# Kernel tuning notes

Hardware: AMD Instinct MI355X
Metric: run time of the kernel (lower is better)

Reference implementation:

```python
import jax, jax.numpy as jnp
import numpy as np

B, N, D = 8, 1024, 512
H, DH = 8, 64          # num_heads, dim_head_output
MLP = 2048
PRUNE_NUM = 64         # remove_num > 0 -> prune branch of determine_fuse
KEEP_NUM = 3
NEG = -1e10


def setup_inputs() -> dict:
    key = jax.random.key(0)
    ks = jax.random.split(key, 10)
    s = 0.02
    inp = {
        "x": jax.random.normal(ks[0], (B, N, D), dtype=jnp.float32),
        "mask": (jax.random.uniform(ks[1], (B, N, N)) < 0.1).astype(jnp.float32),
        "Wqkv": jax.random.normal(ks[2], (D, 3 * H * DH), dtype=jnp.float32) * s,
        "Wout": jax.random.normal(ks[3], (H * DH, D), dtype=jnp.float32) * s,
        "bout": jnp.zeros((D,), jnp.float32),
        "ln1_g": jnp.ones((D,), jnp.float32),
        "ln1_b": jnp.zeros((D,), jnp.float32),
        "ln2_g": jnp.ones((D,), jnp.float32),
        "ln2_b": jnp.zeros((D,), jnp.float32),
        "W1": jax.random.normal(ks[4], (D, MLP), dtype=jnp.float32) * s,
        "b1": jnp.zeros((MLP,), jnp.float32),
        "W2": jax.random.normal(ks[5], (MLP, D), dtype=jnp.float32) * s,
        "b2": jnp.zeros((D,), jnp.float32),
    }
    return inp


def _layer_norm(x, g, b, eps=1e-5):
    mu = jnp.mean(x, axis=-1, keepdims=True)
    var = jnp.mean((x - mu) ** 2, axis=-1, keepdims=True)
    return (x - mu) * jax.lax.rsqrt(var + eps) * g + b


def _attention_with_gos(h, mask, Wqkv, Wout, bout):
    # qkv projection (no bias), chunk into q,k,v then b n (h d) -> b h n d
    qkv = h @ Wqkv                                  # [B,N,3*H*DH]
    q, k, v = jnp.split(qkv, 3, axis=-1)
    def heads(t):
        return t.reshape(B, N, H, DH).transpose(0, 2, 1, 3)  # bhnd
    q, k, v = heads(q), heads(k), heads(v)
    scale = DH ** -0.5
    scores = jnp.einsum("bhnd,bhmd->bhnm", q, k) * scale
    scores = jnp.where(mask[:, None, :, :] == 1.0, NEG, scores)
    attw = jax.nn.softmax(scores, axis=-1)          # [B,H,N,N]
    out = jnp.einsum("bhnm,bhmd->bhnd", attw, v)
    out = out.transpose(0, 2, 1, 3).reshape(B, N, H * DH)
    out = out @ Wout + bout                         # [B,N,D] (dropout=0 -> identity)

    # att_weights_topk = attw.mean(heads)[:, 0]; [:,0] = -inf
    att_topk = attw.mean(axis=1)[:, 0]              # [B,N]
    att_topk = att_topk.at[:, 0].set(-jnp.inf)

    # determine_fuse (prune branch, remove_num > 0)
    nrm = jnp.linalg.norm(out, axis=2, keepdims=True)
    normed = out / jnp.maximum(nrm, 1e-12)          # F.normalize(p=2, dim=2)
    cos = jnp.einsum("bnd,bmd->bnm", normed, normed)
    idx = jnp.arange(N)
    cos = cos.at[:, idx, idx].set(-jnp.inf)
    cos = cos.at[:, 0, :].set(-jnp.inf)
    cos = cos.at[:, :, 0].set(-jnp.inf)
    # NOTE: torch also computes topk of cos.view(B,-1) with k=(N-1)^2, but the
    # result is unused in the remove_num>0 branch (dead code under jit).

    # torch.topk(att_topk, N) sorted descending -> argsort of -att_topk
    attentive_idx = jnp.argsort(-att_topk, axis=1)  # [B,N]
    # pruned = attentive_idx[:, :N-1][:, -PRUNE_NUM:]
    what_to_prune = attentive_idx[:, N - 1 - PRUNE_NUM : N - 1]
    what_to_merge = jnp.full((B, 1), -1, dtype=jnp.int32)
    survived_mask = jnp.zeros((B, 1 + KEEP_NUM, 1 + KEEP_NUM), dtype=jnp.int32)
    return out, what_to_prune, what_to_merge, survived_mask


def reference(x, mask, Wqkv, Wout, bout, ln1_g, ln1_b, ln2_g, ln2_b, W1, b1, W2, b2):
    h = _layer_norm(x, ln1_g, ln1_b)
    att_out, what_to_prune, what_to_merge, survived_mask = _attention_with_gos(
        h, mask, Wqkv, Wout, bout)
    x = x + att_out
    h2 = _layer_norm(x, ln2_g, ln2_b)
    ff = jax.nn.gelu(h2 @ W1 + b1, approximate=False) @ W2 + b2
    x = x + ff
    return x, what_to_prune, what_to_merge, survived_mask
```

## Files before the change

### kernel.cpp

```cpp
#include <hip/hip_runtime.h>
#include <hip/hip_bf16.h>
#include <math.h>

#define BB 8
#define NN 1024
#define DD 512
#define HH 8
#define DHH 64
#define MLPD 2048

typedef __attribute__((ext_vector_type(8))) short short8;
typedef __attribute__((ext_vector_type(4))) float f32x4;

#define MFMA16(a,b,c) __builtin_amdgcn_mfma_f32_16x16x32_bf16(a,b,c,0,0,0)

#define QSCALE 0.18033688011112042f
#define NEGBIG 0xCE6E6B28u

__device__ __forceinline__ short f2bf(float f) {
  union { float f; unsigned u; } x; x.f = f;
  unsigned r = x.u + 0x7FFFu + ((x.u >> 16) & 1u);
  return (short)(r >> 16);
}

__device__ __forceinline__ void gl_lds16(const short* g, short* l) {
  __builtin_amdgcn_global_load_lds(
      (const __attribute__((address_space(1))) unsigned int*)g,
      (__attribute__((address_space(3))) unsigned int*)l, 16, 0, 0);
}

__device__ __forceinline__ float gelu_fast(float t) {
  const float u = 0.7978845608028654f * (t + 0.044715f * t * t * t);
  const float e = __builtin_amdgcn_exp2f(u * 2.8853900817779268f);
  return t - t * __builtin_amdgcn_rcpf(e + 1.0f);
}

template<bool WF32>
__global__ __launch_bounds__(256) void ln_kernel(const float* __restrict__ x,
    const float* __restrict__ gam, const float* __restrict__ bet,
    short* __restrict__ ob, float* __restrict__ of)
{
  const int row = blockIdx.x;
  const int tid = threadIdx.x;
  const float2 xv = *(const float2*)(x + (size_t)row*DD + tid*2);
  double s = (double)xv.x + (double)xv.y;
  for (int o = 32; o >= 1; o >>= 1) s += __shfl_down(s, o, 64);
  __shared__ double red[4];
  const int l = tid & 63, w = tid >> 6;
  if (l == 0) red[w] = s;
  __syncthreads();
  const double mu = (red[0]+red[1]+red[2]+red[3]) * (1.0/512.0);
  const double d0 = (double)xv.x - mu, d1 = (double)xv.y - mu;
  double q = d0*d0 + d1*d1;
  for (int o = 32; o >= 1; o >>= 1) q += __shfl_down(q, o, 64);
  __syncthreads();
  if (l == 0) red[w] = q;
  __syncthreads();
  const double var = (red[0]+red[1]+red[2]+red[3]) * (1.0/512.0);
  const float rs = (float)(1.0 / sqrt(var + 1e-5));
  const float mf = (float)mu;
  const float y0 = (xv.x - mf)*rs*gam[tid*2]   + bet[tid*2];
  const float y1 = (xv.y - mf)*rs*gam[tid*2+1] + bet[tid*2+1];
  ob[(size_t)row*DD + tid*2]   = f2bf(y0);
  ob[(size_t)row*DD + tid*2+1] = f2bf(y1);
  if (WF32) {
    of[(size_t)row*DD + tid*2]   = y0;
    of[(size_t)row*DD + tid*2+1] = y1;
  }
}

__global__ __launch_bounds__(256) void wt_kernel(const float* __restrict__ W,
    short* __restrict__ Wt, int K, int N)
{
  __shared__ float tile[32][33];
  const int n0 = blockIdx.x * 32, k0 = blockIdx.y * 32;
  const int tx = threadIdx.x & 31, ty = threadIdx.x >> 5;
  #pragma unroll
  for (int j = 0; j < 4; j++)
    tile[ty + j*8][tx] = W[(size_t)(k0 + ty + j*8)*N + n0 + tx];
  __syncthreads();
  #pragma unroll
  for (int j = 0; j < 4; j++)
    Wt[(size_t)(n0 + ty + j*8)*K + k0 + tx] = f2bf(tile[tx][ty + j*8]);
}

__global__ __launch_bounds__(256) void maskpack_kernel(const float* __restrict__ mask,
    unsigned long long* __restrict__ mb)
{
  const int wid = blockIdx.x*256 + threadIdx.x;
  if (wid >= BB*NN*16) return;
  const int r = wid >> 4, c = wid & 15;
  const float4* p = (const float4*)(mask + (size_t)r*NN + c*64);
  unsigned long long m = 0;
  #pragma unroll
  for (int i = 0; i < 16; i++) {
    const float4 v = p[i];
    unsigned long long mm = 0;
    if (v.x == 1.0f) mm |= 1ULL;
    if (v.y == 1.0f) mm |= 2ULL;
    if (v.z == 1.0f) mm |= 4ULL;
    if (v.w == 1.0f) mm |= 8ULL;
    m |= mm << (i*4);
  }
  mb[wid] = m;
}

template<int BN, int EPI, int NBUF>
__global__ __launch_bounds__(256) void gemm_bt(
    const short* __restrict__ A, const short* __restrict__ Bt,
    int M, int N, int K,
    const float* __restrict__ bias, const float* __restrict__ res,
    float* __restrict__ outf, short* __restrict__ outb,
    short* __restrict__ outQ, short* __restrict__ outK, short* __restrict__ outVt)
{
  constexpr int CH = 8 + BN/16;
  constexpr int L  = CH/4;
  constexpr int BUFS = (128 + BN)*32;
  __shared__ __align__(16) short lds[NBUF*BUFS];
  const int tid = threadIdx.x;
  const int bm0 = blockIdx.x * 128;
  const int bn0 = blockIdx.y * BN;
  const int lane = tid & 63, wid = tid >> 6;
  const int wm = (wid >> 1) * 64, wn = (wid & 1) * (BN/2);
  const int lr = lane & 15, lg = lane >> 4;
  constexpr int NT = BN/32;

  const short* gsrc[L];
  int loff[L];
  const int scc = (((lane & 3) ^ ((lane >> 3) & 3)))*8;
  #pragma unroll
  for (int i = 0; i < L; i++) {
    const int c = i*4 + wid;
    const int rr = ((c < 8) ? c : c - 8)*16 + (lane >> 2);
    gsrc[i] = (c < 8) ? (A + (size_t)(bm0 + rr)*K + scc)
                      : (Bt + (size_t)(bn0 + rr)*K + scc);
    loff[i] = c*512;
  }
  const int xs = (lr >> 1) & 3;

  f32x4 acc[4][NT];
  #pragma unroll
  for (int i = 0; i < 4; i++)
    #pragma unroll
    for (int j = 0; j < NT; j++) acc[i][j] = f32x4{0.f,0.f,0.f,0.f};

  const int nsteps = K >> 5;

  auto STAGE = [&](int buf, int t) {
    short* dst = lds + buf*BUFS;
    const int ko = t*32;
    #pragma unroll
    for (int i = 0; i < L; i++)
      gl_lds16(gsrc[i] + ko, dst + loff[i]);
  };
  auto COMPUTE = [&](const short* bufA) {
    const short* bufB = bufA + 4096;
    short8 af[4], bfr[NT];
    #pragma unroll
    for (int mt = 0; mt < 4; mt++)
      af[mt] = *(const short8*)(bufA + (wm + mt*16 + lr)*32 + (lg ^ xs)*8);
    #pragma unroll
    for (int nt = 0; nt < NT; nt++)
      bfr[nt] = *(const short8*)(bufB + (wn + nt*16 + lr)*32 + (lg ^ xs)*8);
    __builtin_amdgcn_s_setprio(1);
    #pragma unroll
    for (int mt = 0; mt < 4; mt++)
      #pragma unroll
      for (int nt = 0; nt < NT; nt++)
        acc[mt][nt] = MFMA16(af[mt], bfr[nt], acc[mt][nt]);
    __builtin_amdgcn_s_setprio(0);
  };

  if constexpr (NBUF == 2) {
    STAGE(0, 0);
    asm volatile("s_waitcnt vmcnt(0)" ::: "memory");
    __builtin_amdgcn_s_barrier();
    int cur = 0;
    #pragma unroll 1
    for (int t = 0; t < nsteps; t++) {
      if (t + 1 < nsteps) STAGE(cur ^ 1, t + 1);
      COMPUTE(lds + cur*BUFS);
      asm volatile("s_waitcnt vmcnt(0)" ::: "memory");
      __builtin_amdgcn_s_barrier();
      cur ^= 1;
    }
  } else {
    STAGE(0, 0);
    STAGE(1, 1);
    int cur = 0;
    #pragma unroll 1
    for (int t = 0; t < nsteps; t++) {
      if (t == nsteps - 1) {
        asm volatile("s_waitcnt vmcnt(0)" ::: "memory");
      } else if constexpr (L == 4) {
        asm volatile("s_waitcnt vmcnt(4)" ::: "memory");
      } else {
        asm volatile("s_waitcnt vmcnt(3)" ::: "memory");
      }
      __builtin_amdgcn_s_barrier();
      if (t + 2 < nsteps) {
        const int bnext = (cur == 0) ? 2 : cur - 1;
        STAGE(bnext, t + 2);
      }
      COMPUTE(lds + cur*BUFS);
      cur = (cur == 2) ? 0 : cur + 1;
    }
  }

  if (EPI == 0 && bn0 >= 1024) {
    #pragma unroll
    for (int mt = 0; mt < 4; mt++)
      #pragma unroll
      for (int nt = 0; nt < NT; nt++) {
        const int row0 = bm0 + wm + mt*16 + lg*4;
        const int b = row0 >> 10, tok0 = row0 & 1023;
        const int c2 = bn0 + wn + nt*16 + lr - 1024;
        const int h = c2 >> 6, d = c2 & 63;
        unsigned lo2, hi2;
        asm("v_cvt_pk_bf16_f32 %0, %1, %2" : "=v"(lo2)
            : "v"(acc[mt][nt][0]), "v"(acc[mt][nt][1]));
        asm("v_cvt_pk_bf16_f32 %0, %1, %2" : "=v"(hi2)
            : "v"(acc[mt][nt][2]), "v"(acc[mt][nt][3]));
        uint2 pw; pw.x = lo2; pw.y = hi2;
        *(uint2*)(outVt + (((size_t)(b*HH + h))*DHH + d)*NN + tok0) = pw;
      }
    return;
  }

  #pragma unroll
  for (int mt = 0; mt < 4; mt++)
    #pragma unroll
    for (int nt = 0; nt < NT; nt++)
      #pragma unroll
      for (int r = 0; r < 4; r++) {
        const int row = bm0 + wm + mt*16 + lg*4 + r;
        const int col = bn0 + wn + nt*16 + lr;
        const float v = acc[mt][nt][r];
        if (EPI == 0) {
          const int b = row >> 10, tok = row & 1023;
          if (col < 512) {
            const int h = col >> 6, d = col & 63;
            outQ[(((size_t)(b*HH + h))*NN + tok)*DHH + d] = f2bf(v * QSCALE);
          } else {
            const int c2 = col - 512, h = c2 >> 6, d = c2 & 63;
            outK[(((size_t)(b*HH + h))*NN + tok)*DHH + d] = f2bf(v);
          }
        } else if (EPI == 1) {
          outf[(size_t)row*N + col] = v + bias[col] + res[(size_t)row*N + col];
        } else {
          outb[(size_t)row*N + col] = f2bf(gelu_fast(v + bias[col]));
        }
      }
}

__global__ __launch_bounds__(256) void attn_kernel(
    const short* __restrict__ Qg, const short* __restrict__ Kg,
    const short* __restrict__ Vtg, const unsigned long long* __restrict__ mb,
    short* __restrict__ attout)
{
  const int id = blockIdx.x;
  const int bh = (id & 7)*8 + ((id >> 3) & 7);
  const int qb = id >> 6;
  const int b = bh >> 3, h = bh & 7;
  const int tid = threadIdx.x, lane = tid & 63, w = tid >> 6;
  const int lr = lane & 15, lg = lane >> 4;

  __shared__ __align__(16) short K0[64*64], K1[64*64];
  __shared__ __align__(16) short V0[64*64], V1[64*64];
  __shared__ __align__(16) short PsA[4][16*72], PsB[4][16*72];

  const int qA = qb*128 + w*32 + lr;
  const int qB = qA + 16;
  short* PsAw = &PsA[w][0];
  short* PsBw = &PsB[w][0];

  const size_t qbase = (size_t)bh*NN*DHH;
  const short8 bqA0 = *(const short8*)(Qg + qbase + (size_t)qA*DHH + lg*8);
  const short8 bqA1 = *(const short8*)(Qg + qbase + (size_t)qA*DHH + 32 + lg*8);
  const short8 bqB0 = *(const short8*)(Qg + qbase + (size_t)qB*DHH + lg*8);
  const short8 bqB1 = *(const short8*)(Qg + qbase + (size_t)qB*DHH + 32 + lg*8);

  const unsigned long long* mrowA = mb + ((size_t)b*NN + qA)*16;
  const unsigned long long* mrowB = mb + ((size_t)b*NN + qB)*16;

  const int l8 = lane >> 3;
  const int uu = (lane & 7) ^ l8;
  const short* kgA = Kg + ((size_t)bh*NN + w*16 + l8)*64 + uu*8;
  const short* kgB = kgA + 8*64;
  const short* vgA = Vtg + ((size_t)bh*DHH + w*16 + l8)*NN + uu*8;
  const short* vgB = vgA + 8*NN;
  auto STAGE = [&](short* kb, short* vb, int kc) {
    gl_lds16(kgA + kc*4096, kb + (w*16)*64);
    gl_lds16(kgB + kc*4096, kb + (w*16 + 8)*64);
    gl_lds16(vgA + kc*64,   vb + (w*16)*64);
    gl_lds16(vgB + kc*64,   vb + (w*16 + 8)*64);
  };
  const int xo0 = ((lg ^ (lr & 7)))*8;
  const int xo1 = (((lg ^ (lr & 7))) ^ 4)*8;

  unsigned long long mAc, mBc, mAn, mBn;

  STAGE(K0, V0, 0);
  mAc = mrowA[0]; mBc = mrowB[0];
  asm volatile("s_waitcnt vmcnt(0)" ::: "memory");
  __builtin_amdgcn_s_barrier();

  f32x4 oA[4], oB[4];
  #pragma unroll
  for (int dt = 0; dt < 4; dt++) { oA[dt] = f32x4{0.f,0.f,0.f,0.f}; oB[dt] = f32x4{0.f,0.f,0.f,0.f}; }
  float lsumA = 0.f, lsumB = 0.f;

#define ATT_BODY(CK, CV, NK, NV, MAc, MBc, MAn, MBn, KC, LAST)                 \
  {                                                                            \
    if (!(LAST)) {                                                             \
      STAGE(NK, NV, (KC)+1);                                                   \
      MAn = mrowA[(KC)+1]; MBn = mrowB[(KC)+1];                                \
    }                                                                          \
                              \
    f32x4 sA[4], sB[4];                                                        \
    {                                                                          \
      const unsigned long long mqA = MAc >> (lg*4);                            \
      const unsigned loA = (unsigned)mqA, hiA = (unsigned)(mqA >> 32);         \
      const unsigned long long mqB = MBc >> (lg*4);                            \
      const unsigned loB = (unsigned)mqB, hiB = (unsigned)(mqB >> 32);         \
      _Pragma("unroll")                                                        \
      for (int nt = 0; nt < 4; nt++) {                                         \
        const unsigned wA = (nt < 2) ? loA : hiA;                              \
        const unsigned wB = (nt < 2) ? loB : hiB;                              \
        const int sh = (nt & 1) * 16;                                          \
        _Pragma("unroll")                                                      \
        for (int rr = 0; rr < 4; rr++) {                                       \
          const unsigned bA = (wA >> (sh + rr)) & 1u;                          \
          const unsigned bB = (wB >> (sh + rr)) & 1u;                          \
          sA[nt][rr] = __uint_as_float((0u - bA) & NEGBIG);                    \
          sB[nt][rr] = __uint_as_float((0u - bB) & NEGBIG);                    \
        }                                                                      \
      }                                                                        \
    }                                                                          \
    __builtin_amdgcn_s_setprio(1);                                             \
    _Pragma("unroll")                                                          \
    for (int nt = 0; nt < 4; nt++) {                                           \
      const short* kr = (CK) + (nt*16 + lr)*64;                                \
      const short8 ak0 = *(const short8*)(kr + xo0);                           \
      const short8 ak1 = *(const short8*)(kr + xo1);                           \
      sA[nt] = MFMA16(ak0, bqA0, sA[nt]);                                      \
      sA[nt] = MFMA16(ak1, bqA1, sA[nt]);                                      \
      sB[nt] = MFMA16(ak0, bqB0, sB[nt]);                                      \
      sB[nt] = MFMA16(ak1, bqB1, sB[nt]);                                      \
    }                                                                          \
    __builtin_amdgcn_s_setprio(0);                                             \
    _Pragma("unroll")                                                          \
    for (int nt = 0; nt < 4; nt++) {                                           \
      const float a0 = __builtin_amdgcn_exp2f(sA[nt][0]);                      \
      const float a1 = __builtin_amdgcn_exp2f(sA[nt][1]);                      \
      const float a2 = __builtin_amdgcn_exp2f(sA[nt][2]);                      \
      const float a3 = __builtin_amdgcn_exp2f(sA[nt][3]);                      \
      lsumA += (a0 + a1) + (a2 + a3);                                          \
      unsigned plo, phi;                                                       \
      asm("v_cvt_pk_bf16_f32 %0, %1, %2" : "=v"(plo) : "v"(a0), "v"(a1));      \
      asm("v_cvt_pk_bf16_f32 %0, %1, %2" : "=v"(phi) : "v"(a2), "v"(a3));      \
      uint2 pw; pw.x = plo; pw.y = phi;                                        \
      *(uint2*)(PsAw + lr*72 + nt*16 + lg*4) = pw;                             \
      const float c0 = __builtin_amdgcn_exp2f(sB[nt][0]);                      \
      const float c1 = __builtin_amdgcn_exp2f(sB[nt][1]);                      \
      const float c2 = __builtin_amdgcn_exp2f(sB[nt][2]);                      \
      const float c3 = __builtin_amdgcn_exp2f(sB[nt][3]);                      \
      lsumB += (c0 + c1) + (c2 + c3);                                          \
      unsigned qlo, qhi;                                                       \
      asm("v_cvt_pk_bf16_f32 %0, %1, %2" : "=v"(qlo) : "v"(c0), "v"(c1));      \
      asm("v_cvt_pk_bf16_f32 %0, %1, %2" : "=v"(qhi) : "v"(c2), "v"(c3));      \
      uint2 qw; qw.x = qlo; qw.y = qhi;                                        \
      *(uint2*)(PsBw + lr*72 + nt*16 + lg*4) = qw;                             \
    }                                                                          \
    {                                                                          \
      const short8 bpA0 = *(const short8*)(PsAw + lr*72 + lg*8);               \
      const short8 bpA1 = *(const short8*)(PsAw + lr*72 + 32 + lg*8);          \
      const short8 bpB0 = *(const short8*)(PsBw + lr*72 + lg*8);               \
      const short8 bpB1 = *(const short8*)(PsBw + lr*72 + 32 + lg*8);          \
      __builtin_amdgcn_s_setprio(1);                                           \
      _Pragma("unroll")                                                        \
      for (int dt = 0; dt < 4; dt++) {                                         \
        const short* vr = (CV) + (dt*16 + lr)*64;                              \
        const short8 av0 = *(const short8*)(vr + xo0);                         \
        const short8 av1 = *(const short8*)(vr + xo1);                         \
        oA[dt] = MFMA16(av0, bpA0, oA[dt]);                                    \
        oA[dt] = MFMA16(av1, bpA1, oA[dt]);                                    \
        oB[dt] = MFMA16(av0, bpB0, oB[dt]);                                    \
        oB[dt] = MFMA16(av1, bpB1, oB[dt]);                                    \
      }                                                                        \
      __builtin_amdgcn_s_setprio(0);                                           \
    }                                                                          \
    if (!(LAST)) {                                                             \
      asm volatile("s_waitcnt vmcnt(0)" ::: "memory");                         \
      __builtin_amdgcn_s_barrier();                                            \
      MAc = MAn; MBc = MBn;                                                    \
    }                                                                          \
  }

  #pragma unroll 1
  for (int kc = 0; kc < 16; kc += 2) {
    ATT_BODY(K0, V0, K1, V1, mAc, mBc, mAn, mBn, kc, false)
    ATT_BODY(K1, V1, K0, V0, mAc, mBc, mAn, mBn, kc+1, (kc+1) == 15)
  }
#undef ATT_BODY

  lsumA += __shfl_xor(lsumA, 16, 64);
  lsumA += __shfl_xor(lsumA, 32, 64);
  lsumB += __shfl_xor(lsumB, 16, 64);
  lsumB += __shfl_xor(lsumB, 32, 64);
  const float linvA = 1.0f / lsumA;
  const float linvB = 1.0f / lsumB;

  #pragma unroll
  for (int dt = 0; dt < 4; dt++) {
    unsigned w0, w1, w2, w3;
    const float a0 = oA[dt][0]*linvA, a1 = oA[dt][1]*linvA;
    const float a2 = oA[dt][2]*linvA, a3 = oA[dt][3]*linvA;
    asm("v_cvt_pk_bf16_f32 %0, %1, %2" : "=v"(w0) : "v"(a0), "v"(a1));
    asm("v_cvt_pk_bf16_f32 %0, %1, %2" : "=v"(w1) : "v"(a2), "v"(a3));
    uint2 ow; ow.x = w0; ow.y = w1;
    *(uint2*)(PsAw + lr*72 + dt*16 + lg*4) = ow;
    const float c0 = oB[dt][0]*linvB, c1 = oB[dt][1]*linvB;
    const float c2 = oB[dt][2]*linvB, c3 = oB[dt][3]*linvB;
    asm("v_cvt_pk_bf16_f32 %0, %1, %2" : "=v"(w2) : "v"(c0), "v"(c1));
    asm("v_cvt_pk_bf16_f32 %0, %1, %2" : "=v"(w3) : "v"(c2), "v"(c3));
    uint2 ow2; ow2.x = w2; ow2.y = w3;
    *(uint2*)(PsBw + lr*72 + dt*16 + lg*4) = ow2;
  }
  #pragma unroll
  for (int rep = 0; rep < 2; rep++) {
    const int c = lane + rep*64;
    const int row = c >> 3, off = c & 7;
    const uint4 ovA = *(const uint4*)(PsAw + row*72 + off*8);
    *(uint4*)(attout + ((size_t)b*NN + qb*128 + w*32 + row)*DD + h*DHH + off*8) = ovA;
    const uint4 ovB = *(const uint4*)(PsBw + row*72 + off*8);
    *(uint4*)(attout + ((size_t)b*NN + qb*128 + w*32 + 16 + row)*DD + h*DHH + off*8) = ovB;
  }
}

__global__ __launch_bounds__(512) void q0_kernel(const float* __restrict__ hlnf,
    const float* __restrict__ Wqkv, double* __restrict__ q0)
{
  const int bh = blockIdx.x, b = bh >> 3, h = bh & 7;
  const int d = threadIdx.x & 63, cg = threadIdx.x >> 6;
  double acc = 0.0;
  #pragma unroll 8
  for (int c = cg*64; c < cg*64 + 64; c++)
    acc += (double)hlnf[(size_t)b*NN*DD + c] * (double)Wqkv[(size_t)c*1536 + h*64 + d];
  __shared__ double red[512];
  red[threadIdx.x] = acc;
  __syncthreads();
  if (threadIdx.x < 64) {
    double s = 0.0;
    #pragma unroll
    for (int g = 0; g < 8; g++) s += red[g*64 + d];
    q0[bh*64 + d] = s;
  }
}

__global__ __launch_bounds__(512) void wv_kernel(const float* __restrict__ Wqkv,
    const double* __restrict__ q0, double* __restrict__ wv)
{
  const int bh = blockIdx.x, h = bh & 7;
  __shared__ double q0s[64];
  if (threadIdx.x < 64) q0s[threadIdx.x] = q0[bh*64 + threadIdx.x];
  __syncthreads();
  const int c = threadIdx.x;
  const float4* wp = (const float4*)(Wqkv + (size_t)c*1536 + 512 + h*64);
  double acc = 0.0;
  #pragma unroll
  for (int dv = 0; dv < 16; dv++) {
    const float4 wq = wp[dv];
    acc += q0s[dv*4+0]*(double)wq.x + q0s[dv*4+1]*(double)wq.y
         + q0s[dv*4+2]*(double)wq.z + q0s[dv*4+3]*(double)wq.w;
  }
  wv[(size_t)bh*512 + c] = acc;
}

__global__ __launch_bounds__(256) void srow_kernel(const float* __restrict__ hlnf,
    const double* __restrict__ wv, const float* __restrict__ mask,
    double* __restrict__ srow)
{
  const int b = blockIdx.x, jc = blockIdx.y;
  const int jl = threadIdx.x >> 3;
  const int cg = threadIdx.x & 7;
  const int j  = jc*32 + jl;
  __shared__ double lw[8*512];
  __shared__ double red[32][8][9];
  for (int i = threadIdx.x; i < 4096; i += 256) lw[i] = wv[(size_t)b*4096 + i];
  __syncthreads();
  double acc[8] = {0,0,0,0,0,0,0,0};
  const float* xr = hlnf + ((size_t)b*NN + j)*DD;
  #pragma unroll
  for (int i = 0; i < 16; i++) {
    const int c = cg*4 + i*32;
    const float4 xv4 = *(const float4*)(xr + c);
    #pragma unroll
    for (int h = 0; h < 8; h++) {
      const double* lwc = lw + h*512 + c;
      acc[h] += (double)xv4.x*lwc[0] + (double)xv4.y*lwc[1]
              + (double)xv4.z*lwc[2] + (double)xv4.w*lwc[3];
    }
  }
  #pragma unroll
  for (int h = 0; h < 8; h++) red[jl][cg][h] = acc[h];
  __syncthreads();
  const int j2 = threadIdx.x >> 3, h2 = threadIdx.x & 7;
  double s = 0.0;
  #pragma unroll
  for (int g = 0; g < 8; g++) s += red[j2][g][h2];
  s *= 0.125;
  const float mval = mask[(size_t)b*NN*NN + jc*32 + j2];
  if (mval == 1.0f) s = -1e10;
  srow[((size_t)b*8 + h2)*NN + jc*32 + j2] = s;
}

__global__ __launch_bounds__(256) void msum_kernel(const double* __restrict__ srow,
    double* __restrict__ ms)
{
  const int bh = blockIdx.x;
  const double* s = srow + (size_t)bh*NN;
  double mx = -1e300;
  for (int j = threadIdx.x; j < NN; j += 256) mx = fmax(mx, s[j]);
  for (int o = 32; o >= 1; o >>= 1) mx = fmax(mx, __shfl_xor(mx, o, 64));
  __shared__ double red[4];
  if ((threadIdx.x & 63) == 0) red[threadIdx.x >> 6] = mx;
  __syncthreads();
  mx = fmax(fmax(red[0], red[1]), fmax(red[2], red[3]));
  double sum = 0.0;
  for (int j = threadIdx.x; j < NN; j += 256) sum += exp(s[j] - mx);
  for (int o = 32; o >= 1; o >>= 1) sum += __shfl_xor(sum, o, 64);
  __syncthreads();
  if ((threadIdx.x & 63) == 0) red[threadIdx.x >> 6] = sum;
  __syncthreads();
  if (threadIdx.x == 0) { ms[bh*2] = mx; ms[bh*2+1] = red[0]+red[1]+red[2]+red[3]; }
}

__global__ __launch_bounds__(1024) void sort_kernel(const double* __restrict__ srow,
    const double* __restrict__ ms, float* __restrict__ dout,
    int offP, int offM, int offS)
{
  const int b = blockIdx.x;
  const int j = threadIdx.x;
  __shared__ double vals[1024];
  __shared__ int    idx[1024];
  double a;
  if (j == 0) a = -INFINITY;
  else {
    double t = 0.0;
    #pragma unroll
    for (int h = 0; h < 8; h++) {
      const double m  = ms[(b*8 + h)*2];
      const double su = ms[(b*8 + h)*2 + 1];
      t += exp(srow[((size_t)b*8 + h)*NN + j] - m) / su;
    }
    a = t * 0.125;
  }
  vals[j] = a; idx[j] = j;
  for (int k = 2; k <= 1024; k <<= 1)
    for (int jj = k >> 1; jj > 0; jj >>= 1) {
      __syncthreads();
      const int ixj = j ^ jj;
      if (ixj > j) {
        const double v1 = vals[j], v2 = vals[ixj];
        const int i1 = idx[j], i2 = idx[ixj];
        const bool less12 = (v1 > v2) || (v1 == v2 && i1 < i2);
        const bool up = ((j & k) == 0);
        if (up ? !less12 : less12) {
          vals[j] = v2; vals[ixj] = v1; idx[j] = i2; idx[ixj] = i1;
        }
      }
    }
  __syncthreads();
  if (j >= 959 && j <= 1022) dout[offP + b*64 + (j - 959)] = (float)idx[j];
  if (b == 0) {
    if (j < 8)   dout[offM + j] = -1.0f;
    if (j < 128) dout[offS + j] = 0.0f;
  }
}

extern "C" void kernel_launch(void* const* d_in, const int* in_sizes, int n_in,
                              void* d_out, int out_size, void* d_ws, size_t ws_size,
                              hipStream_t stream) {
  (void)in_sizes; (void)n_in; (void)out_size; (void)ws_size;
  const float* x     = (const float*)d_in[0];
  const float* mask  = (const float*)d_in[1];
  const float* Wqkv  = (const float*)d_in[2];
  const float* Wout  = (const float*)d_in[3];
  const float* bout  = (const float*)d_in[4];
  const float* ln1g  = (const float*)d_in[5];
  const float* ln1b  = (const float*)d_in[6];
  const float* ln2g  = (const float*)d_in[7];
  const float* ln2b  = (const float*)d_in[8];
  const float* W1    = (const float*)d_in[9];
  const float* b1    = (const float*)d_in[10];
  const float* W2    = (const float*)d_in[11];
  const float* b2    = (const float*)d_in[12];
  float* dout = (float*)d_out;

  const size_t MB = 1ull << 20;
  char* ws = (char*)d_ws;
  short*  hln_bf = (short*)(ws + 0);
  float*  hlnf   = (float*)(ws + 8*MB);
  short*  Qg     = (short*)(ws + 24*MB);
  short*  Kg     = (short*)(ws + 32*MB);
  short*  Vtg    = (short*)(ws + 40*MB);
  unsigned long long* mbits = (unsigned long long*)(ws + 48*MB);
  short*  Wqkvt  = (short*)(ws + 49*MB);
  short*  Woutt  = (short*)(ws + 51*MB);
  short*  W1t    = (short*)(ws + 52*MB);
  short*  W2t    = (short*)(ws + 54*MB);
  double* q0v    = (double*)(ws + 56*MB);
  double* wvv    = (double*)(ws + 56*MB + 256*1024);
  double* srow   = (double*)(ws + 57*MB);
  double* msv    = (double*)(ws + 58*MB);
  short*  attout = (short*)(ws + 60*MB);
  float*  x1     = (float*)(ws + 68*MB);
  short*  h2     = (short*)(ws + 84*MB);
  short*  gbuf   = (short*)(ws + 0);

  const int offP = BB*NN*DD;
  const int offM = offP + BB*64;
  const int offS = offM + BB;

  ln_kernel<true><<<BB*NN, 256, 0, stream>>>(x, ln1g, ln1b, hln_bf, hlnf);

  q0_kernel<<<BB*HH, 512, 0, stream>>>(hlnf, Wqkv, q0v);
  wv_kernel<<<BB*HH, 512, 0, stream>>>(Wqkv, q0v, wvv);
  srow_kernel<<<dim3(BB, 32), 256, 0, stream>>>(hlnf, wvv, mask, srow);
  msum_kernel<<<BB*HH, 256, 0, stream>>>(srow, msv);
  sort_kernel<<<BB, 1024, 0, stream>>>(srow, msv, dout, offP, offM, offS);

  maskpack_kernel<<<(BB*NN*16)/256, 256, 0, stream>>>(mask, mbits);
  wt_kernel<<<dim3(1536/32, 512/32),  256, 0, stream>>>(Wqkv, Wqkvt, 512, 1536);
  wt_kernel<<<dim3(512/32, 512/32),   256, 0, stream>>>(Wout, Woutt, 512, 512);
  wt_kernel<<<dim3(2048/32, 512/32),  256, 0, stream>>>(W1,   W1t,   512, 2048);
  wt_kernel<<<dim3(512/32, 2048/32),  256, 0, stream>>>(W2,   W2t,   2048, 512);

  gemm_bt<128,0,3><<<dim3(64, 12), 256, 0, stream>>>(hln_bf, Wqkvt, BB*NN, 1536, 512,
      nullptr, nullptr, nullptr, nullptr, Qg, Kg, Vtg);

  attn_kernel<<<512, 256, 0, stream>>>(Qg, Kg, Vtg, mbits, attout);

  gemm_bt<64,1,3><<<dim3(64, 8), 256, 0, stream>>>(attout, Woutt, BB*NN, 512, 512,
      bout, x, x1, nullptr, nullptr, nullptr, nullptr);

  ln_kernel<false><<<BB*NN, 256, 0, stream>>>(x1, ln2g, ln2b, h2, nullptr);

  gemm_bt<128,2,2><<<dim3(64, 16), 256, 0, stream>>>(h2, W1t, BB*NN, 2048, 512,
      b1, nullptr, nullptr, gbuf, nullptr, nullptr, nullptr);

  gemm_bt<64,1,3><<<dim3(64, 8), 256, 0, stream>>>(gbuf, W2t, BB*NN, 512, 2048,
      b2, x1, dout, nullptr, nullptr, nullptr, nullptr);
}
```

Baseline: 212.2 us.

## Merge small setup kernels and replace bitonic sort with parallel rank selection

Four weight-transpose launches are folded into one launch that dispatches tiles by block index, and the q0 and wv kernels are fused so q0 stays in shared memory. The single-block-per-batch bitonic sort is replaced by a rank kernel over 32 blocks, where each thread counts how many elements beat its value and writes the pruned index directly. This cuts launch count and the long serial sync chain of the sort, at the cost of O(N^2) comparisons per batch and recomputing attention averages in every slab.

```diff
diff --git a/kernel.cpp b/kernel.cpp
--- a/kernel.cpp
+++ b/kernel.cpp
@@ -69,11 +69,21 @@
   }
 }
 
-__global__ __launch_bounds__(256) void wt_kernel(const float* __restrict__ W,
-    short* __restrict__ Wt, int K, int N)
-{
+__global__ __launch_bounds__(256) void wtall_kernel(
+    const float* __restrict__ Wqkv, const float* __restrict__ Wout,
+    const float* __restrict__ W1,   const float* __restrict__ W2,
+    short* __restrict__ Wqkvt, short* __restrict__ Woutt,
+    short* __restrict__ W1t,   short* __restrict__ W2t)
+{
+  const int id = blockIdx.x;
+  const float* W; short* Wt; int K, N, t;
+  if (id < 768)       { W = Wqkv; Wt = Wqkvt; K = 512;  N = 1536; t = id; }
+  else if (id < 1024) { W = Wout; Wt = Woutt; K = 512;  N = 512;  t = id - 768; }
+  else if (id < 2048) { W = W1;   Wt = W1t;   K = 512;  N = 2048; t = id - 1024; }
+  else                { W = W2;   Wt = W2t;   K = 2048; N = 512;  t = id - 2048; }
+  const int nx = N >> 5;
+  const int n0 = (t % nx)*32, k0 = (t / nx)*32;
   __shared__ float tile[32][33];
-  const int n0 = blockIdx.x * 32, k0 = blockIdx.y * 32;
   const int tx = threadIdx.x & 31, ty = threadIdx.x >> 5;
   #pragma unroll
   for (int j = 0; j < 4; j++)
@@ -438,33 +448,28 @@
   }
 }
 
-__global__ __launch_bounds__(512) void q0_kernel(const float* __restrict__ hlnf,
-    const float* __restrict__ Wqkv, double* __restrict__ q0)
+__global__ __launch_bounds__(512) void q0wv_kernel(const float* __restrict__ hlnf,
+    const float* __restrict__ Wqkv, double* __restrict__ wv)
 {
   const int bh = blockIdx.x, b = bh >> 3, h = bh & 7;
-  const int d = threadIdx.x & 63, cg = threadIdx.x >> 6;
-  double acc = 0.0;
-  #pragma unroll 8
-  for (int c = cg*64; c < cg*64 + 64; c++)
-    acc += (double)hlnf[(size_t)b*NN*DD + c] * (double)Wqkv[(size_t)c*1536 + h*64 + d];
   __shared__ double red[512];
-  red[threadIdx.x] = acc;
-  __syncthreads();
-  if (threadIdx.x < 64) {
-    double s = 0.0;
-    #pragma unroll
-    for (int g = 0; g < 8; g++) s += red[g*64 + d];
-    q0[bh*64 + d] = s;
-  }
-}
-
-__global__ __launch_bounds__(512) void wv_kernel(const float* __restrict__ Wqkv,
-    const double* __restrict__ q0, double* __restrict__ wv)
-{
-  const int bh = blockIdx.x, h = bh & 7;
   __shared__ double q0s[64];
-  if (threadIdx.x < 64) q0s[threadIdx.x] = q0[bh*64 + threadIdx.x];
-  __syncthreads();
+  {
+    const int d = threadIdx.x & 63, cg = threadIdx.x >> 6;
+    double acc = 0.0;
+    #pragma unroll 8
+    for (int c = cg*64; c < cg*64 + 64; c++)
+      acc += (double)hlnf[(size_t)b*NN*DD + c] * (double)Wqkv[(size_t)c*1536 + h*64 + d];
+    red[threadIdx.x] = acc;
+    __syncthreads();
+    if (threadIdx.x < 64) {
+      double s = 0.0;
+      #pragma unroll
+      for (int g = 0; g < 8; g++) s += red[g*64 + d];
+      q0s[d] = s;
+    }
+    __syncthreads();
+  }
   const int c = threadIdx.x;
   const float4* wp = (const float4*)(Wqkv + (size_t)c*1536 + 512 + h*64);
   double acc = 0.0;
@@ -536,46 +541,43 @@
   if (threadIdx.x == 0) { ms[bh*2] = mx; ms[bh*2+1] = red[0]+red[1]+red[2]+red[3]; }
 }
 
-__global__ __launch_bounds__(1024) void sort_kernel(const double* __restrict__ srow,
+__global__ __launch_bounds__(256) void rank_kernel(const double* __restrict__ srow,
     const double* __restrict__ ms, float* __restrict__ dout,
     int offP, int offM, int offS)
 {
-  const int b = blockIdx.x;
-  const int j = threadIdx.x;
-  __shared__ double vals[1024];
-  __shared__ int    idx[1024];
-  double a;
-  if (j == 0) a = -INFINITY;
-  else {
-    double t = 0.0;
-    #pragma unroll
-    for (int h = 0; h < 8; h++) {
-      const double m  = ms[(b*8 + h)*2];
-      const double su = ms[(b*8 + h)*2 + 1];
-      t += exp(srow[((size_t)b*8 + h)*NN + j] - m) / su;
+  const int b = blockIdx.x, slab = blockIdx.y;
+  const int t = threadIdx.x;
+  __shared__ double a[1024];
+  #pragma unroll
+  for (int rep = 0; rep < 4; rep++) {
+    const int k = rep*256 + t;
+    double att;
+    if (k == 0) att = -INFINITY;
+    else {
+      double s = 0.0;
+      #pragma unroll
+      for (int h = 0; h < 8; h++) {
+        const double m  = ms[(b*8 + h)*2];
+        const double su = ms[(b*8 + h)*2 + 1];
+        s += exp(srow[((size_t)b*8 + h)*NN + k] - m) / su;
+      }
+      att = s * 0.125;
     }
-    a = t * 0.125;
-  }
-  vals[j] = a; idx[j] = j;
-  for (int k = 2; k <= 1024; k <<= 1)
-    for (int jj = k >> 1; jj > 0; jj >>= 1) {
-      __syncthreads();
-      const int ixj = j ^ jj;
-      if (ixj > j) {
-        const double v1 = vals[j], v2 = vals[ixj];
-        const int i1 = idx[j], i2 = idx[ixj];
-        const bool less12 = (v1 > v2) || (v1 == v2 && i1 < i2);
-        const bool up = ((j & k) == 0);
-        if (up ? !less12 : less12) {
-          vals[j] = v2; vals[ixj] = v1; idx[j] = i2; idx[ixj] = i1;
-        }
-      }
-    }
-  __syncthreads();
-  if (j >= 959 && j <= 1022) dout[offP + b*64 + (j - 959)] = (float)idx[j];
-  if (b == 0) {
-    if (j < 8)   dout[offM + j] = -1.0f;
-    if (j < 128) dout[offS + j] = 0.0f;
+    a[k] = att;
+  }
+  __syncthreads();
+  const int j = slab*256 + t;
+  const double aj = a[j];
+  int r = 0;
+  #pragma unroll 8
+  for (int k = 0; k < 1024; k++) {
+    const double ak = a[k];
+    r += ((ak > aj) || (ak == aj && k < j)) ? 1 : 0;
+  }
+  if (r >= 959 && r <= 1022) dout[offP + b*64 + (r - 959)] = (float)j;
+  if (b == 0 && slab == 0) {
+    if (t < 8)   dout[offM + t] = -1.0f;
+    if (t < 128) dout[offS + t] = 0.0f;
   }
 }
 
@@ -610,7 +612,6 @@
   short*  Woutt  = (short*)(ws + 51*MB);
   short*  W1t    = (short*)(ws + 52*MB);
   short*  W2t    = (short*)(ws + 54*MB);
-  double* q0v    = (double*)(ws + 56*MB);
   double* wvv    = (double*)(ws + 56*MB + 256*1024);
   double* srow   = (double*)(ws + 57*MB);
   double* msv    = (double*)(ws + 58*MB);
@@ -625,17 +626,14 @@
 
   ln_kernel<true><<<BB*NN, 256, 0, stream>>>(x, ln1g, ln1b, hln_bf, hlnf);
 
-  q0_kernel<<<BB*HH, 512, 0, stream>>>(hlnf, Wqkv, q0v);
-  wv_kernel<<<BB*HH, 512, 0, stream>>>(Wqkv, q0v, wvv);
+  q0wv_kernel<<<BB*HH, 512, 0, stream>>>(hlnf, Wqkv, wvv);
   srow_kernel<<<dim3(BB, 32), 256, 0, stream>>>(hlnf, wvv, mask, srow);
   msum_kernel<<<BB*HH, 256, 0, stream>>>(srow, msv);
-  sort_kernel<<<BB, 1024, 0, stream>>>(srow, msv, dout, offP, offM, offS);
+  rank_kernel<<<dim3(BB, 4), 256, 0, stream>>>(srow, msv, dout, offP, offM, offS);
 
   maskpack_kernel<<<(BB*NN*16)/256, 256, 0, stream>>>(mask, mbits);
-  wt_kernel<<<dim3(1536/32, 512/32),  256, 0, stream>>>(Wqkv, Wqkvt, 512, 1536);
-  wt_kernel<<<dim3(512/32, 512/32),   256, 0, stream>>>(Wout, Woutt, 512, 512);
-  wt_kernel<<<dim3(2048/32, 512/32),  256, 0, stream>>>(W1,   W1t,   512, 2048);
-  wt_kernel<<<dim3(512/32, 2048/32),  256, 0, stream>>>(W2,   W2t,   2048, 512);
+  wtall_kernel<<<3072, 256, 0, stream>>>(Wqkv, Wout, W1, W2,
+      Wqkvt, Woutt, W1t, W2t);
 
   gemm_bt<128,0,3><<<dim3(64, 12), 256, 0, stream>>>(hln_bf, Wqkvt, BB*NN, 1536, 512,
       nullptr, nullptr, nullptr, nullptr, Qg, Kg, Vtg);
```

New measurement: 224.1 us. 1.06x slower.
